# Kernel optimization log

Measured on AMD Instinct MI355X. Metric: run time of the kernel, lower is better.

The kernel has to match this reference:

```python
import jax, jax.numpy as jnp
import numpy as np

N, IN_DIM, HID, M, T, E, A, OUT = 10000, 256, 256, 8, 3, 160000, 2000, 10
LN_EPS = 1e-5


def _layernorm(x, g, b):
    mu = x.mean(-1, keepdims=True)
    var = ((x - mu) ** 2).mean(-1, keepdims=True)
    return (x - mu) * jax.lax.rsqrt(var + LN_EPS) * g + b


def _gcn_conv(x, w, b, src, dst, n):
    # PyG GCNConv: x' = D^{-1/2}(A+I)D^{-1/2} (x W) + b, deg counted on dst with self-loops
    xw = x @ w  # [n, out]
    loops = jnp.arange(n, dtype=src.dtype)
    s = jnp.concatenate([src, loops])
    d = jnp.concatenate([dst, loops])
    deg = jax.ops.segment_sum(jnp.ones(d.shape[0], xw.dtype), d, num_segments=n)
    dinv = jax.lax.rsqrt(jnp.maximum(deg, 1.0))
    norm = dinv[s] * dinv[d]
    out = jax.ops.segment_sum(xw[s] * norm[:, None], d, num_segments=n)
    return out + b


def setup_inputs() -> dict:
    key = jax.random.key(0)
    ks = jax.random.split(key, 26)
    g = lambda i, shape: (jax.random.normal(ks[i], shape, jnp.float32) * 0.02)
    return {
        "edge_index_t": jax.random.randint(ks[0], (T, 2, E), 0, N),
        "node_t": jax.random.randint(ks[1], (T, A), 0, N),
        "m": M,
        "emb": g(2, (N, IN_DIM)),
        "gcn_w1": g(3, (IN_DIM, HID)), "gcn_b1": jnp.zeros((HID,), jnp.float32),
        "gcn_w2": g(4, (HID, HID)), "gcn_b2": jnp.zeros((HID,), jnp.float32),
        "ln1_g": jnp.ones((HID,), jnp.float32), "ln1_b": jnp.zeros((HID,), jnp.float32),
        "tok_w1": g(5, (M, M)), "tok_b1": jnp.zeros((M,), jnp.float32),
        "tok_w2": g(6, (M, M)), "tok_b2": jnp.zeros((M,), jnp.float32),
        "ln2_g": jnp.ones((HID,), jnp.float32), "ln2_b": jnp.zeros((HID,), jnp.float32),
        "ch_w1": g(7, (HID, HID)), "ch_b1": jnp.zeros((HID,), jnp.float32),
        "ch_w2": g(8, (HID, HID)), "ch_b2": jnp.zeros((HID,), jnp.float32),
        "pred_w": g(9, (HID, HID)), "pred_b": jnp.zeros((HID,), jnp.float32),
        "cls1_w": g(10, (HID, HID)), "cls1_b": jnp.zeros((HID,), jnp.float32),
        "cls2_w": g(11, (HID, OUT)), "cls2_b": jnp.zeros((OUT,), jnp.float32),
    }


def reference(edge_index_t, node_t, m, emb,
              gcn_w1, gcn_b1, gcn_w2, gcn_b2,
              ln1_g, ln1_b, tok_w1, tok_b1, tok_w2, tok_b2,
              ln2_g, ln2_b, ch_w1, ch_b1, ch_w2, ch_b2,
              pred_w, pred_b, cls1_w, cls1_b, cls2_w, cls2_b):
    n = emb.shape[0]

    def mixer(xm):  # [n, m, hid]
        y = _layernorm(xm, ln1_g, ln1_b)
        # token MLP over the m axis (transpose(1,2) in torch)
        y = jnp.einsum('nmh,mk->nkh', y, tok_w1) + tok_b1[None, :, None]
        y = jax.nn.gelu(y, approximate=False)
        y = jnp.einsum('nmh,mk->nkh', y, tok_w2) + tok_b2[None, :, None]
        x = xm + y
        z = _layernorm(x, ln2_g, ln2_b)
        z = jax.nn.gelu(z @ ch_w1 + ch_b1, approximate=False) @ ch_w2 + ch_b2
        return x + z

    def step(x_m, inp):
        src, dst, nid = inp
        # forecast from current window (before this step's graph update)
        x_new = mixer(x_m).mean(axis=1)  # discrete FinalProcessLayer: mean over tokens
        # 2-layer GCN on the (shared) initial embeddings
        x = _gcn_conv(emb, gcn_w1, gcn_b1, src, dst, n)
        x = jax.nn.relu(x)
        x = _gcn_conv(x, gcn_w2, gcn_b2, src, dst, n)
        # boolean-mask scatter: zero rows of nodes listed in node_t[i]
        x = x.at[nid].set(0.0)
        x_m = jnp.concatenate([x_m[:, 1:, :], x[:, None, :]], axis=1)
        return x_m, x_new

    x_m0 = jnp.zeros((n, m, HID), emb.dtype)
    _, v = jax.lax.scan(step, x_m0, (edge_index_t[:, 0], edge_index_t[:, 1], node_t))
    # InvariantPredictor over all T timesteps at once: v [T, n, hid]
    h = jnp.tanh(v @ pred_w + pred_b)
    y_hat = jax.nn.relu((h @ cls1_w + cls1_b) @ cls2_w + cls2_b)
    return h, y_hat
```

## Files before the change

### kernel.cpp

```cpp
#include <hip/hip_runtime.h>
#include <math.h>

#define NN 10000
#define HIDD 256
#define MTOK 8
#define TT 3
#define EE 160000
#define AA 2000
#define OUTD 10
#define LNEPS 1e-5f

typedef unsigned short u16;
typedef __attribute__((ext_vector_type(8))) __bf16 bf16x8;
typedef __attribute__((ext_vector_type(4))) float f32x4;

__device__ __forceinline__ float gelu_f(float x) {
    return 0.5f * x * (1.f + erff(x * 0.7071067811865475f));
}
__device__ __forceinline__ u16 f2bf(float x) {
    unsigned u = __builtin_bit_cast(unsigned, x);
    return (u16)((u + 0x7FFFu + ((u >> 16) & 1u)) >> 16);
}
__device__ __forceinline__ float bf2f(u16 b) {
    return __builtin_bit_cast(float, (unsigned)b << 16);
}
__device__ __forceinline__ void gload16(const void* g, void* l) {
    __builtin_amdgcn_global_load_lds(
        (const __attribute__((address_space(1))) unsigned int*)g,
        (__attribute__((address_space(3))) unsigned int*)l, 16, 0, 0);
}

__global__ void count_kernel(const int* __restrict__ edge, int* __restrict__ cnt) {
    int g = blockIdx.y;
    const int* dst = edge + (size_t)g * 2 * EE + EE;
    int e = blockIdx.x * 256 + threadIdx.x;
    if (e < EE) atomicAdd(&cnt[g * NN + dst[e]], 1);
}

__global__ __launch_bounds__(1024) void scan_kernel(const int* __restrict__ cnt_all,
        int* __restrict__ rowstart_all, int* __restrict__ cursor_all, float* __restrict__ dinv_all) {
    int g = blockIdx.x;
    const int* cnt = cnt_all + (size_t)g * NN;
    int* rowstart = rowstart_all + (size_t)g * NN;
    int* cursor = cursor_all + (size_t)g * NN;
    float* dinv = dinv_all + (size_t)g * NN;
    __shared__ int wsum[16];
    int tid = threadIdx.x, lane = tid & 63, wid = tid >> 6;
    int carry = 0;
    for (int base = 0; base < NN; base += 1024) {
        int i = base + tid;
        int v = (i < NN) ? cnt[i] : 0;
        int s = v;
        #pragma unroll
        for (int o = 1; o < 64; o <<= 1) {
            int t = __shfl_up(s, o, 64);
            if (lane >= o) s += t;
        }
        if (lane == 63) wsum[wid] = s;
        __syncthreads();
        if (wid == 0) {
            int ws = (lane < 16) ? wsum[lane] : 0;
            #pragma unroll
            for (int o = 1; o < 16; o <<= 1) {
                int t = __shfl_up(ws, o, 64);
                if (lane >= o) ws += t;
            }
            if (lane < 16) wsum[lane] = ws;
        }
        __syncthreads();
        int woff = (wid > 0) ? wsum[wid - 1] : 0;
        int tot = wsum[15];
        if (i < NN) {
            int excl = carry + s + woff - v;
            rowstart[i] = excl;
            cursor[i] = excl;
            dinv[i] = rsqrtf((float)(v + 1));
        }
        carry += tot;
        __syncthreads();
    }
}

__global__ void fill_kernel(const int* __restrict__ edge, int* __restrict__ cursor, int* __restrict__ esrc) {
    int g = blockIdx.y;
    const int* src = edge + (size_t)g * 2 * EE;
    const int* dst = src + EE;
    int e = blockIdx.x * 256 + threadIdx.x;
    if (e < EE) {
        int d = dst[e];
        int idx = atomicAdd(&cursor[g * NN + d], 1);
        esrc[(size_t)g * EE + idx] = src[e];
    }
}

template<int RELU, int WF32, int WSPLIT>
__global__ __launch_bounds__(256) void gcn_agg(const float* __restrict__ xw, size_t xw_goff,
        const int* __restrict__ esrc_all, const int* __restrict__ rowstart_all,
        const int* __restrict__ cnt_all, const float* __restrict__ dinv_all,
        const float* __restrict__ bias, float* __restrict__ out,
        u16* __restrict__ ohi, u16* __restrict__ olo) {
    int g = blockIdx.y;
    const float* xwg = xw + (size_t)g * xw_goff;
    const int* esrc = esrc_all + (size_t)g * EE;
    const int* rowstart = rowstart_all + (size_t)g * NN;
    const int* cntp = cnt_all + (size_t)g * NN;
    const float* dinv = dinv_all + (size_t)g * NN;
    int wave = threadIdx.x >> 6, lane = threadIdx.x & 63;
    int d = blockIdx.x * 4 + wave;
    if (d >= NN) return;
    int start = rowstart[d];
    int len = cntp[d];
    float dd = dinv[d];
    int h = lane * 4;
    float4 a = *(const float4*)&xwg[(size_t)d * HIDD + h];
    float4 acc;
    acc.x = a.x * dd; acc.y = a.y * dd; acc.z = a.z * dd; acc.w = a.w * dd;
    for (int i = 0; i < len; i++) {
        int s = esrc[start + i];
        float ds = dinv[s];
        float4 b = *(const float4*)&xwg[(size_t)s * HIDD + h];
        acc.x = fmaf(b.x, ds, acc.x);
        acc.y = fmaf(b.y, ds, acc.y);
        acc.z = fmaf(b.z, ds, acc.z);
        acc.w = fmaf(b.w, ds, acc.w);
    }
    float o0 = acc.x * dd + bias[h + 0];
    float o1 = acc.y * dd + bias[h + 1];
    float o2 = acc.z * dd + bias[h + 2];
    float o3 = acc.w * dd + bias[h + 3];
    if (RELU) {
        o0 = fmaxf(o0, 0.f); o1 = fmaxf(o1, 0.f); o2 = fmaxf(o2, 0.f); o3 = fmaxf(o3, 0.f);
    }
    size_t obase = (size_t)g * NN * HIDD + (size_t)d * HIDD + h;
    if (WF32) {
        float4 o; o.x = o0; o.y = o1; o.z = o2; o.w = o3;
        *(float4*)&out[obase] = o;
    }
    if (WSPLIT) {
        ushort4 hv, lv;
        u16 h0 = f2bf(o0), h1 = f2bf(o1), h2 = f2bf(o2), h3 = f2bf(o3);
        hv.x = h0; hv.y = h1; hv.z = h2; hv.w = h3;
        lv.x = f2bf(o0 - bf2f(h0)); lv.y = f2bf(o1 - bf2f(h1));
        lv.z = f2bf(o2 - bf2f(h2)); lv.w = f2bf(o3 - bf2f(h3));
        *(ushort4*)&ohi[obase] = hv;
        *(ushort4*)&olo[obase] = lv;
    }
}

__global__ void mask_kernel(const int* __restrict__ node_t, float* __restrict__ xs) {
    int g = blockIdx.y;
    int node = node_t[(size_t)g * AA + blockIdx.x];
    xs[(size_t)g * NN * HIDD + (size_t)node * HIDD + threadIdx.x] = 0.f;
}

__global__ void split_kernel(const float* __restrict__ x, u16* __restrict__ hi, u16* __restrict__ lo, int n) {
    int i = blockIdx.x * 256 + threadIdx.x;
    if (i < n) {
        float v = x[i];
        u16 h = f2bf(v);
        hi[i] = h;
        lo[i] = f2bf(v - bf2f(h));
    }
}

__global__ void wsplit_all(const float* __restrict__ w0, const float* __restrict__ w1,
        const float* __restrict__ w2, const float* __restrict__ w3,
        const float* __restrict__ w4, const float* __restrict__ w5, u16* __restrict__ bt) {
    const float* W[6] = { w0, w1, w2, w3, w4, w5 };
    const float* Wm = W[blockIdx.y];
    u16* Bt = bt + (size_t)blockIdx.y * 256 * 768;
    int c = blockIdx.x, k = threadIdx.x;
    float x = Wm[k * 256 + c];
    u16 hi = f2bf(x), lo = f2bf(x - bf2f(hi));
    Bt[c * 768 + k] = hi;
    Bt[c * 768 + 256 + k] = hi;
    Bt[c * 768 + 512 + k] = lo;
}

template<int ACT, int WF32, int WSPLIT, int EPI>
__global__ __launch_bounds__(256) void gemm_split(
        const u16* __restrict__ Ahi, const u16* __restrict__ Alo,
        const u16* __restrict__ Bt, const float* __restrict__ bias,
        float* __restrict__ outf, u16* __restrict__ ohi, u16* __restrict__ olo,
        const float* __restrict__ xsum, int R) {
    __shared__ __align__(16) u16 ldsA[3][128 * 64];
    __shared__ __align__(16) u16 ldsB[2][128 * 64];
    int tid = threadIdx.x;
    int lane = tid & 63, w = tid >> 6;
    int nwg = gridDim.x, orig = blockIdx.x;
    int xcd = orig & 7, i8 = orig >> 3;
    int q = nwg >> 3, r = nwg & 7;
    int bid = (xcd < r ? xcd * (q + 1) : r * (q + 1) + (xcd - r) * q) + i8;
    int rowbase = (bid >> 1) * 128;
    int cb = bid & 1;
    int wrow = (w >> 1) * 64, wcol = (w & 1) * 64;
    f32x4 acc[4][4];
    #pragma unroll
    for (int i = 0; i < 4; i++)
        #pragma unroll
        for (int j = 0; j < 4; j++) acc[i][j] = f32x4{0.f, 0.f, 0.f, 0.f};

    constexpr int KCH[12]  = {0,4,1,5,2,6,3,7,8,9,10,11};
    constexpr int BNEW[12] = {1,0,1,0,1,0,1,0,1,1,1,1};
    constexpr int BBUF[12] = {0,0,1,1,0,0,1,1,0,1,0,1};
    constexpr int VMC[12]  = {8,12,8,12,8,12,8,12,12,12,8,0};

    auto stageA = [&](int slot, int c) {
        const u16* Aseg = (c >= 4 && c < 8) ? Alo : Ahi;
        int koff = (c & 3) * 64;
        #pragma unroll
        for (int i = 0; i < 4; i++) {
            int j = i * 256 + tid;
            int rr = j >> 3, sl = j & 7;
            int grow = rowbase + rr; if (grow > R - 1) grow = R - 1;
            const u16* gp = Aseg + (size_t)grow * 256 + koff + ((sl ^ (rr & 7)) << 3);
            gload16(gp, &ldsA[slot][(i * 256 + (tid & 192)) << 3]);
        }
    };
    auto stageB = [&](int buf, int c) {
        #pragma unroll
        for (int i = 0; i < 4; i++) {
            int j = i * 256 + tid;
            int rr = j >> 3, sl = j & 7;
            const u16* gp = Bt + (size_t)(cb * 128 + rr) * 768 + c * 64 + ((sl ^ (rr & 7)) << 3);
            gload16(gp, &ldsB[buf][(i * 256 + (tid & 192)) << 3]);
        }
    };

    stageB(0, KCH[0]);
    stageA(0, KCH[0]);
    stageA(1, KCH[1]);
    #pragma unroll
    for (int p = 0; p < 12; p++) {
        if (p + 1 <= 11 && BNEW[p + 1]) stageB(BBUF[p + 1], KCH[p + 1]);
        if (p + 2 <= 11) stageA((p + 2) % 3, KCH[p + 2]);
        if (VMC[p] == 12)      asm volatile("s_waitcnt vmcnt(12)" ::: "memory");
        else if (VMC[p] == 8)  asm volatile("s_waitcnt vmcnt(8)" ::: "memory");
        else                   asm volatile("s_waitcnt vmcnt(0)" ::: "memory");
        __builtin_amdgcn_s_barrier();
        __builtin_amdgcn_sched_barrier(0);
        __builtin_amdgcn_s_setprio(1);
        #pragma unroll
        for (int ks = 0; ks < 2; ks++) {
            bf16x8 a[4], b[4];
            #pragma unroll
            for (int rf = 0; rf < 4; rf++) {
                int rr = wrow + rf * 16 + (lane & 15);
                int slot = (lane >> 4) + ks * 4;
                a[rf] = *(const bf16x8*)&ldsA[p % 3][(rr << 6) + ((slot ^ (rr & 7)) << 3)];
            }
            #pragma unroll
            for (int cf = 0; cf < 4; cf++) {
                int cc = wcol + cf * 16 + (lane & 15);
                int slot = (lane >> 4) + ks * 4;
                b[cf] = *(const bf16x8*)&ldsB[BBUF[p]][(cc << 6) + ((slot ^ (cc & 7)) << 3)];
            }
            #pragma unroll
            for (int rf = 0; rf < 4; rf++)
                #pragma unroll
                for (int cf = 0; cf < 4; cf++)
                    acc[rf][cf] = __builtin_amdgcn_mfma_f32_16x16x32_bf16(a[rf], b[cf], acc[rf][cf], 0, 0, 0);
        }
        __builtin_amdgcn_s_setprio(0);
        __builtin_amdgcn_sched_barrier(0);
        __builtin_amdgcn_s_barrier();
    }
    #pragma unroll
    for (int rf = 0; rf < 4; rf++) {
        #pragma unroll
        for (int cf = 0; cf < 4; cf++) {
            int col = cb * 128 + wcol + cf * 16 + (lane & 15);
            float bv = bias[col];
            f32x4 v = acc[rf][cf];
            if (EPI == 1) {
                float s = 0.f;
                #pragma unroll
                for (int r2 = 0; r2 < 4; r2++) s += gelu_f(v[r2] + bv);
                float o = __shfl_xor(s, 16, 64);
                float nodesum = s + o;
                if (((lane >> 4) & 1) == 0) {
                    int node = ((rowbase + wrow + rf * 16) >> 3) + ((lane >> 4) >> 1);
                    u16 hi = f2bf(nodesum), lo = f2bf(nodesum - bf2f(hi));
                    ohi[(size_t)node * 256 + col] = hi;
                    olo[(size_t)node * 256 + col] = lo;
                }
            } else if (EPI == 2) {
                int row0 = rowbase + wrow + rf * 16 + ((lane >> 4) << 2);
                #pragma unroll
                for (int r2 = 0; r2 < 4; r2++) {
                    int row = row0 + r2;
                    if (row < R) {
                        float val = (xsum[(size_t)row * 256 + col] + v[r2] + 8.f * bv) * 0.125f;
                        u16 hi = f2bf(val), lo = f2bf(val - bf2f(hi));
                        ohi[(size_t)row * 256 + col] = hi;
                        olo[(size_t)row * 256 + col] = lo;
                    }
                }
            } else {
                int row0 = rowbase + wrow + rf * 16 + ((lane >> 4) << 2);
                #pragma unroll
                for (int r2 = 0; r2 < 4; r2++) {
                    int row = row0 + r2;
                    if (row < R) {
                        float val = v[r2] + bv;
                        if (ACT == 1) val = gelu_f(val);
                        if (ACT == 2) val = tanhf(val);
                        if (WF32) outf[(size_t)row * 256 + col] = val;
                        if (WSPLIT) {
                            u16 hi = f2bf(val), lo = f2bf(val - bf2f(hi));
                            ohi[(size_t)row * 256 + col] = hi;
                            olo[(size_t)row * 256 + col] = lo;
                        }
                    }
                }
            }
        }
    }
}

__global__ __launch_bounds__(256) void mixer_front(
        const float* __restrict__ xs, int nodebase,
        const float* __restrict__ ln1_g, const float* __restrict__ ln1_b,
        const float* __restrict__ tw1, const float* __restrict__ tb1,
        const float* __restrict__ tw2, const float* __restrict__ tb2,
        const float* __restrict__ ln2_g, const float* __restrict__ ln2_b,
        u16* __restrict__ z_hi, u16* __restrict__ z_lo, float* __restrict__ xsum_out) {
    int nv = nodebase + blockIdx.x;
    int step = nv >= NN ? 1 : 0;
    int n = nv - step * NN;
    const float* p1 = xs + ((size_t)step * NN + n) * HIDD;
    const float* p2 = step ? xs + (size_t)n * HIDD : nullptr;
    int tid = threadIdx.x;
    int wave = tid >> 6, lane = tid & 63;
    __shared__ __align__(16) float sx[MTOK][HIDD];
    __shared__ float stw1h[16], stw2[64], stb1[8], stb2[8], sw1s6[8];
    __shared__ float red[MTOK][2];
    if (tid < 16) stw1h[tid] = tw1[48 + tid];
    if (tid < 64) stw2[tid] = tw2[tid];
    if (tid < 8) {
        stb1[tid] = tb1[tid]; stb2[tid] = tb2[tid];
        float s = 0.f;
        #pragma unroll
        for (int m = 0; m < 6; m++) s += tw1[m * MTOK + tid];
        sw1s6[tid] = s;
    }
    sx[6][tid] = p2 ? p2[tid] : 0.f;
    sx[7][tid] = p1[tid];
    __syncthreads();
    float g1v = ln1_g[tid], b1v = ln1_b[tid];
    if (wave < 2) {
        int m = 6 + wave;
        float x0 = sx[m][lane], x1 = sx[m][lane + 64], x2 = sx[m][lane + 128], x3 = sx[m][lane + 192];
        float s = x0 + x1 + x2 + x3;
        float ss = x0 * x0 + x1 * x1 + x2 * x2 + x3 * x3;
        for (int off = 32; off > 0; off >>= 1) { s += __shfl_down(s, off, 64); ss += __shfl_down(ss, off, 64); }
        if (lane == 0) {
            float mu = s * (1.f / HIDD);
            float var = ss * (1.f / HIDD) - mu * mu;
            red[m][0] = mu;
            red[m][1] = rsqrtf(var + LNEPS);
        }
    }
    __syncthreads();
    float x6 = sx[6][tid], x7 = sx[7][tid];
    float ty6 = (x6 - red[6][0]) * red[6][1] * g1v + b1v;
    float ty7 = (x7 - red[7][0]) * red[7][1] * g1v + b1v;
    float u[MTOK];
    #pragma unroll
    for (int k = 0; k < MTOK; k++) {
        float a = stb1[k];
        a = fmaf(b1v, sw1s6[k], a);
        a = fmaf(ty6, stw1h[k], a);
        a = fmaf(ty7, stw1h[8 + k], a);
        u[k] = gelu_f(a);
    }
    float xsm = 0.f;
    #pragma unroll
    for (int k = 0; k < MTOK; k++) {
        float a = stb2[k];
        #pragma unroll
        for (int m = 0; m < MTOK; m++) a = fmaf(u[m], stw2[m * MTOK + k], a);
        if (k == 6) a += x6;
        if (k == 7) a += x7;
        sx[k][tid] = a;
        xsm += a;
    }
    xsum_out[(size_t)nv * HIDD + tid] = xsm;
    __syncthreads();
    float g2v = ln2_g[tid], b2v = ln2_b[tid];
    #pragma unroll
    for (int rep = 0; rep < 2; rep++) {
        int m = wave + rep * 4;
        float x0 = sx[m][lane], x1 = sx[m][lane + 64], x2 = sx[m][lane + 128], x3 = sx[m][lane + 192];
        float s = x0 + x1 + x2 + x3;
        float ss = x0 * x0 + x1 * x1 + x2 * x2 + x3 * x3;
        for (int off = 32; off > 0; off >>= 1) { s += __shfl_down(s, off, 64); ss += __shfl_down(ss, off, 64); }
        if (lane == 0) {
            float mu = s * (1.f / HIDD);
            float var = ss * (1.f / HIDD) - mu * mu;
            red[m][0] = mu;
            red[m][1] = rsqrtf(var + LNEPS);
        }
    }
    __syncthreads();
    #pragma unroll
    for (int m = 0; m < MTOK; m++) {
        float z = (sx[m][tid] - red[m][0]) * red[m][1] * g2v + b2v;
        u16 hi = f2bf(z), lo = f2bf(z - bf2f(hi));
        size_t idx = ((size_t)blockIdx.x * MTOK + m) * HIDD + tid;
        z_hi[idx] = hi;
        z_lo[idx] = lo;
    }
}

__global__ __launch_bounds__(256) void mixer_kernel(
        const float* __restrict__ ln1_g, const float* __restrict__ ln1_b,
        const float* __restrict__ tw1, const float* __restrict__ tb1,
        const float* __restrict__ tw2, const float* __restrict__ tb2,
        const float* __restrict__ ln2_g, const float* __restrict__ ln2_b,
        const float* __restrict__ cw1, const float* __restrict__ cb1,
        const float* __restrict__ cw2, const float* __restrict__ cb2,
        float* __restrict__ vout) {
    int tid = threadIdx.x;
    __shared__ __align__(16) float sx[MTOK][HIDD];
    __shared__ __align__(16) float sy[MTOK][HIDD];
    __shared__ float stw1[64], stw2[64], stb1[8], stb2[8];
    if (tid < 64) { stw1[tid] = tw1[tid]; stw2[tid] = tw2[tid]; }
    if (tid < 8)  { stb1[tid] = tb1[tid]; stb2[tid] = tb2[tid]; }
    __syncthreads();
    float b1v = ln1_b[tid];
    float ty[MTOK];
    #pragma unroll
    for (int m = 0; m < MTOK; m++) ty[m] = b1v;
    float u[MTOK];
    #pragma unroll
    for (int k = 0; k < MTOK; k++) {
        float a = stb1[k];
        #pragma unroll
        for (int m = 0; m < MTOK; m++) a = fmaf(ty[m], stw1[m * MTOK + k], a);
        u[k] = gelu_f(a);
    }
    #pragma unroll
    for (int k = 0; k < MTOK; k++) {
        float a = stb2[k];
        #pragma unroll
        for (int m = 0; m < MTOK; m++) a = fmaf(u[m], stw2[m * MTOK + k], a);
        sx[k][tid] = a;
    }
    __syncthreads();
    __shared__ float red[MTOK][2];
    int wave = tid >> 6, lane = tid & 63;
    float g2v = ln2_g[tid], b2v = ln2_b[tid];
    #pragma unroll
    for (int rep = 0; rep < 2; rep++) {
        int m = wave + rep * 4;
        float x0 = sx[m][lane], x1 = sx[m][lane + 64], x2 = sx[m][lane + 128], x3 = sx[m][lane + 192];
        float s = x0 + x1 + x2 + x3;
        float ss = x0 * x0 + x1 * x1 + x2 * x2 + x3 * x3;
        for (int off = 32; off > 0; off >>= 1) { s += __shfl_down(s, off, 64); ss += __shfl_down(ss, off, 64); }
        if (lane == 0) {
            float mu = s * (1.f / HIDD);
            float var = ss * (1.f / HIDD) - mu * mu;
            red[m][0] = mu;
            red[m][1] = rsqrtf(var + LNEPS);
        }
    }
    __syncthreads();
    #pragma unroll
    for (int m = 0; m < MTOK; m++) sy[m][tid] = (sx[m][tid] - red[m][0]) * red[m][1] * g2v + b2v;
    __syncthreads();
    float acc[MTOK];
    #pragma unroll
    for (int m = 0; m < MTOK; m++) acc[m] = 0.f;
    for (int h = 0; h < HIDD; h += 4) {
        float w0 = cw1[(h + 0) * HIDD + tid];
        float w1 = cw1[(h + 1) * HIDD + tid];
        float w2 = cw1[(h + 2) * HIDD + tid];
        float w3 = cw1[(h + 3) * HIDD + tid];
        #pragma unroll
        for (int m = 0; m < MTOK; m++) {
            const float4 a = *(const float4*)&sy[m][h];
            acc[m] = fmaf(a.x, w0, acc[m]);
            acc[m] = fmaf(a.y, w1, acc[m]);
            acc[m] = fmaf(a.z, w2, acc[m]);
            acc[m] = fmaf(a.w, w3, acc[m]);
        }
    }
    __syncthreads();
    float cb1v = cb1[tid];
    #pragma unroll
    for (int m = 0; m < MTOK; m++) sy[m][tid] = gelu_f(acc[m] + cb1v);
    __syncthreads();
    float acc2[MTOK];
    #pragma unroll
    for (int m = 0; m < MTOK; m++) acc2[m] = 0.f;
    for (int h = 0; h < HIDD; h += 4) {
        float w0 = cw2[(h + 0) * HIDD + tid];
        float w1 = cw2[(h + 1) * HIDD + tid];
        float w2 = cw2[(h + 2) * HIDD + tid];
        float w3 = cw2[(h + 3) * HIDD + tid];
        #pragma unroll
        for (int m = 0; m < MTOK; m++) {
            const float4 a = *(const float4*)&sy[m][h];
            acc2[m] = fmaf(a.x, w0, acc2[m]);
            acc2[m] = fmaf(a.y, w1, acc2[m]);
            acc2[m] = fmaf(a.z, w2, acc2[m]);
            acc2[m] = fmaf(a.w, w3, acc2[m]);
        }
    }
    float cb2v = cb2[tid];
    float ssum = 0.f;
    #pragma unroll
    for (int m = 0; m < MTOK; m++) ssum += sx[m][tid] + acc2[m] + cb2v;
    vout[tid] = ssum * (1.f / MTOK);
}

__global__ __launch_bounds__(256) void t0_head(const float* __restrict__ v0row,
        const float* __restrict__ pred_w, const float* __restrict__ pred_b,
        const float* __restrict__ cls1_w, const float* __restrict__ cls1_b,
        const float* __restrict__ cls2_w, const float* __restrict__ cls2_b,
        float* __restrict__ h0row, float* __restrict__ y0row) {
    __shared__ float s[HIDD], s2[HIDD];
    int tid = threadIdx.x;
    s[tid] = v0row[tid];
    __syncthreads();
    float a = 0.f;
    for (int k = 0; k < HIDD; k++) a = fmaf(s[k], pred_w[k * HIDD + tid], a);
    float h = tanhf(a + pred_b[tid]);
    h0row[tid] = h;
    s2[tid] = h;
    __syncthreads();
    a = 0.f;
    for (int k = 0; k < HIDD; k++) a = fmaf(s2[k], cls1_w[k * HIDD + tid], a);
    float g = a + cls1_b[tid];
    __syncthreads();
    s[tid] = g;
    __syncthreads();
    if (tid < OUTD) {
        float y = 0.f;
        for (int k = 0; k < HIDD; k++) y = fmaf(s[k], cls2_w[k * OUTD + tid], y);
        y0row[tid] = fmaxf(y + cls2_b[tid], 0.f);
    }
}

__global__ void bcast_both(const float* __restrict__ h0row, const float* __restrict__ y0row,
        float* __restrict__ hout, float* __restrict__ yout) {
    int n = blockIdx.x, tid = threadIdx.x;
    hout[(size_t)n * HIDD + tid] = h0row[tid];
    if (tid < OUTD) yout[(size_t)n * OUTD + tid] = y0row[tid];
}

__global__ __launch_bounds__(256) void cls2_kernel(const float* __restrict__ g1, const float* __restrict__ wm,
        const float* __restrict__ b, float* __restrict__ out, int rows) {
    __shared__ float sw[HIDD][12];
    int tid = threadIdx.x;
    for (int i = tid; i < HIDD * OUTD; i += 256) sw[i / OUTD][i % OUTD] = wm[i];
    __syncthreads();
    int rl = tid >> 4, kk = tid & 15;
    int r = blockIdx.x * 16 + rl;
    if (r < rows && kk < OUTD) {
        float acc = 0.f;
        const float* grow = g1 + (size_t)r * HIDD;
        for (int h = 0; h < HIDD; h++) acc = fmaf(grow[h], sw[h][kk], acc);
        out[(size_t)r * OUTD + kk] = fmaxf(acc + b[kk], 0.f);
    }
}

extern "C" void kernel_launch(void* const* d_in, const int* in_sizes, int n_in,
                              void* d_out, int out_size, void* d_ws, size_t ws_size,
                              hipStream_t stream) {
    const int* edge    = (const int*)d_in[0];
    const int* node_t  = (const int*)d_in[1];
    const float* emb   = (const float*)d_in[3];
    const float* gcn_w1 = (const float*)d_in[4];
    const float* gcn_b1 = (const float*)d_in[5];
    const float* gcn_w2 = (const float*)d_in[6];
    const float* gcn_b2 = (const float*)d_in[7];
    const float* ln1_g = (const float*)d_in[8];
    const float* ln1_b = (const float*)d_in[9];
    const float* tw1   = (const float*)d_in[10];
    const float* tb1   = (const float*)d_in[11];
    const float* tw2   = (const float*)d_in[12];
    const float* tb2   = (const float*)d_in[13];
    const float* ln2_g = (const float*)d_in[14];
    const float* ln2_b = (const float*)d_in[15];
    const float* cw1   = (const float*)d_in[16];
    const float* cb1   = (const float*)d_in[17];
    const float* cw2   = (const float*)d_in[18];
    const float* cb2   = (const float*)d_in[19];
    const float* pred_w = (const float*)d_in[20];
    const float* pred_b = (const float*)d_in[21];
    const float* cls1_w = (const float*)d_in[22];
    const float* cls1_b = (const float*)d_in[23];
    const float* cls2_w = (const float*)d_in[24];
    const float* cls2_b = (const float*)d_in[25];

    const size_t NH = (size_t)NN * HIDD;
    char* wsb = (char*)d_ws;
    size_t off = 0;
    auto alloc = [&](size_t bytes) { char* p = wsb + off; off = (off + bytes + 255) & ~(size_t)255; return p; };
    float* xs   = (float*)alloc(2 * NH * 4);
    u16* v_hi   = (u16*)alloc(2 * NH * 2);
    u16* v_lo   = (u16*)alloc(2 * NH * 2);
    u16* h_hi   = (u16*)alloc(2 * NH * 2);
    u16* h_lo   = (u16*)alloc(2 * NH * 2);
    float* xw2  = (float*)alloc(2 * NH * 4);
    float* xsum = (float*)alloc(2 * NH * 4);
    u16* Bt_all = (u16*)alloc((size_t)6 * 256 * 768 * 2);
    u16* Bt_cw1  = Bt_all;
    u16* Bt_cw2  = Bt_all + 1 * 256 * 768;
    u16* Bt_pred = Bt_all + 2 * 256 * 768;
    u16* Bt_cls1 = Bt_all + 3 * 256 * 768;
    u16* Bt_gw1  = Bt_all + 4 * 256 * 768;
    u16* Bt_gw2  = Bt_all + 5 * 256 * 768;
    float* dinv  = (float*)alloc(2 * NN * 4);
    float* zeros = (float*)alloc(HIDD * 4);
    float* v0row = (float*)alloc(HIDD * 4);
    float* h0row = (float*)alloc(HIDD * 4);
    float* y0row = (float*)alloc(16 * 4);
    int* cnt    = (int*)alloc(2 * NN * 4);
    int* rowst  = (int*)alloc(2 * NN * 4);
    int* cursor = (int*)alloc(2 * NN * 4);
    int* esrc   = (int*)alloc((size_t)2 * EE * 4);
    float* xw    = (float*)h_hi;
    u16*  emb_hi = h_lo;
    u16*  emb_lo = h_lo + NH;
    u16*  agg_hi = v_hi;
    u16*  agg_lo = v_lo;
    u16*  s2_hi  = (u16*)xw2;
    u16*  s2_lo  = (u16*)xw2 + 2 * NH;
    float* g1    = xw2;
    size_t remain = (ws_size > off + 4096) ? (ws_size - off - 4096) : 0;
    int CHN = (int)(remain / 8192);
    if (CHN > 2 * NN) CHN = 2 * NN;
    CHN &= ~15;
    if (CHN < 16) CHN = 16;
    const size_t ZE = (size_t)CHN * MTOK * HIDD;
    u16* z_hi  = (u16*)alloc(ZE * 2);
    u16* z_lo  = (u16*)alloc(ZE * 2);

    float* h_out = (float*)d_out;
    float* y_out = h_out + (size_t)TT * NH;

    hipMemsetAsync(zeros, 0, HIDD * sizeof(float), stream);
    wsplit_all<<<dim3(256, 6), 256, 0, stream>>>(cw1, cw2, pred_w, cls1_w, gcn_w1, gcn_w2, Bt_all);
    split_kernel<<<(NN * HIDD + 255) / 256, 256, 0, stream>>>(emb, emb_hi, emb_lo, NN * HIDD);
    gemm_split<0, 1, 0, 0><<<2 * ((NN + 127) / 128), 256, 0, stream>>>(
        emb_hi, emb_lo, Bt_gw1, zeros, xw, nullptr, nullptr, nullptr, NN);

    mixer_kernel<<<1, 256, 0, stream>>>(ln1_g, ln1_b, tw1, tb1, tw2, tb2,
        ln2_g, ln2_b, cw1, cb1, cw2, cb2, v0row);
    t0_head<<<1, 256, 0, stream>>>(v0row, pred_w, pred_b, cls1_w, cls1_b,
        cls2_w, cls2_b, h0row, y0row);
    bcast_both<<<NN, 256, 0, stream>>>(h0row, y0row, h_out, y_out);

    hipMemsetAsync(cnt, 0, 2 * NN * sizeof(int), stream);
    count_kernel<<<dim3((EE + 255) / 256, 2), 256, 0, stream>>>(edge, cnt);
    scan_kernel<<<2, 1024, 0, stream>>>(cnt, rowst, cursor, dinv);
    fill_kernel<<<dim3((EE + 255) / 256, 2), 256, 0, stream>>>(edge, cursor, esrc);
    gcn_agg<1, 0, 1><<<dim3((NN + 3) / 4, 2), 256, 0, stream>>>(xw, 0,
        esrc, rowst, cnt, dinv, gcn_b1, nullptr, agg_hi, agg_lo);
    gemm_split<0, 1, 0, 0><<<2 * ((2 * NN + 127) / 128), 256, 0, stream>>>(
        agg_hi, agg_lo, Bt_gw2, zeros, xw2, nullptr, nullptr, nullptr, 2 * NN);
    gcn_agg<0, 1, 0><<<dim3((NN + 3) / 4, 2), 256, 0, stream>>>(xw2, NH,
        esrc, rowst, cnt, dinv, gcn_b2, xs, nullptr, nullptr);
    mask_kernel<<<dim3(AA, 2), 256, 0, stream>>>(node_t, xs);

    for (int nb = 0; nb < 2 * NN; nb += CHN) {
        int nodes = 2 * NN - nb < CHN ? 2 * NN - nb : CHN;
        int R = nodes * MTOK;
        int rb = (R + 127) / 128;
        mixer_front<<<nodes, 256, 0, stream>>>(xs, nb,
            ln1_g, ln1_b, tw1, tb1, tw2, tb2, ln2_g, ln2_b, z_hi, z_lo, xsum);
        gemm_split<1, 0, 0, 1><<<2 * rb, 256, 0, stream>>>(
            z_hi, z_lo, Bt_cw1, cb1, nullptr,
            s2_hi + (size_t)nb * HIDD, s2_lo + (size_t)nb * HIDD, nullptr, R);
    }
    gemm_split<0, 0, 0, 2><<<2 * ((2 * NN + 127) / 128), 256, 0, stream>>>(
        s2_hi, s2_lo, Bt_cw2, cb2, nullptr, v_hi, v_lo, xsum, 2 * NN);
    gemm_split<2, 1, 1, 0><<<2 * ((2 * NN + 127) / 128), 256, 0, stream>>>(
        v_hi, v_lo, Bt_pred, pred_b,
        h_out + NH, h_hi, h_lo, nullptr, 2 * NN);
    gemm_split<0, 1, 0, 0><<<2 * ((2 * NN + 127) / 128), 256, 0, stream>>>(
        h_hi, h_lo, Bt_cls1, cls1_b, g1, nullptr, nullptr, nullptr, 2 * NN);
    cls2_kernel<<<(2 * NN + 15) / 16, 256, 0, stream>>>(g1, cls2_w, cls2_b, y_out + (size_t)NN * OUTD, 2 * NN);
}
```

Measured before the change: 550.6 us.

## Fuse channel-mix second GEMM, predictor, and classifier into one tail kernel

Replaces the last four launches (cw2 GEMM with mean epilogue, pred GEMM with tanh, cls1 GEMM, cls2 matvec) with one kernel. Each 64-row block keeps its activation tile in LDS as split bf16 hi/lo and chains the three 256x256 GEMMs while streaming weight chunks through double-buffered LDS. The cls2 projection then runs from LDS. This removes the global round trips for the intermediate activations and three launches. In exchange it uses large LDS (one block per CU), a smaller row tile, and recomputes weight staging per block.

```diff
diff --git a/kernel.cpp b/kernel.cpp
--- a/kernel.cpp
+++ b/kernel.cpp
@@ -284,18 +284,6 @@
                     ohi[(size_t)node * 256 + col] = hi;
                     olo[(size_t)node * 256 + col] = lo;
                 }
-            } else if (EPI == 2) {
-                int row0 = rowbase + wrow + rf * 16 + ((lane >> 4) << 2);
-                #pragma unroll
-                for (int r2 = 0; r2 < 4; r2++) {
-                    int row = row0 + r2;
-                    if (row < R) {
-                        float val = (xsum[(size_t)row * 256 + col] + v[r2] + 8.f * bv) * 0.125f;
-                        u16 hi = f2bf(val), lo = f2bf(val - bf2f(hi));
-                        ohi[(size_t)row * 256 + col] = hi;
-                        olo[(size_t)row * 256 + col] = lo;
-                    }
-                }
             } else {
                 int row0 = rowbase + wrow + rf * 16 + ((lane >> 4) << 2);
                 #pragma unroll
@@ -314,6 +302,132 @@
                     }
                 }
             }
+        }
+    }
+}
+
+__global__ __launch_bounds__(512, 1) void tail_fused(
+        const u16* __restrict__ s2_hi, const u16* __restrict__ s2_lo,
+        const float* __restrict__ xsum,
+        const u16* __restrict__ Bt_cw2, const float* __restrict__ cb2,
+        const u16* __restrict__ Bt_pred, const float* __restrict__ pred_b,
+        const u16* __restrict__ Bt_cls1, const float* __restrict__ cls1_b,
+        const float* __restrict__ cls2_w, const float* __restrict__ cls2_b,
+        float* __restrict__ h_out1, float* __restrict__ y_out1, int R) {
+    __shared__ __align__(16) u16 ldsA[2][64 * 256];
+    __shared__ __align__(16) u16 ldsB[2][256 * 64];
+    int tid = threadIdx.x;
+    int lane = tid & 63, wid = tid >> 6;
+    int wrow = (wid & 3) * 16, wcol = (wid >> 2) * 128;
+    int rowbase = blockIdx.x * 64;
+
+    constexpr int KCH[12]  = {0,4,1,5,2,6,3,7,8,9,10,11};
+    constexpr int BNEW[12] = {1,0,1,0,1,0,1,0,1,1,1,1};
+    constexpr int BBUF[12] = {0,0,1,1,0,0,1,1,0,1,0,1};
+
+    auto stageB = [&](int buf, int c, const u16* Bt) {
+        #pragma unroll
+        for (int i = 0; i < 4; i++) {
+            int j = i * 512 + tid;
+            int cc = j >> 3, sl = j & 7;
+            const u16* gp = Bt + (size_t)cc * 768 + c * 64 + ((sl ^ (cc & 7)) << 3);
+            gload16(gp, &ldsB[buf][(i * 512 + (tid & 448)) << 3]);
+        }
+    };
+    #pragma unroll
+    for (int seg = 0; seg < 2; seg++) {
+        const u16* src = seg ? s2_lo : s2_hi;
+        #pragma unroll
+        for (int i = 0; i < 4; i++) {
+            int j = i * 512 + tid;
+            int rr = j >> 5;
+            int gch = (j >> 3) & 3, t = j & 7;
+            int rowG = rowbase + rr; if (rowG > R - 1) rowG = R - 1;
+            const u16* gp = src + (size_t)rowG * 256 + gch * 64 + ((t ^ (rr & 7)) << 3);
+            gload16(gp, &ldsA[seg][(i * 512 + (tid & 448)) << 3]);
+        }
+    }
+
+    const u16* Bts0 = Bt_cw2;
+    const u16* Bts1 = Bt_pred;
+    const u16* Bts2 = Bt_cls1;
+    for (int s = 0; s < 3; s++) {
+        const u16* Bt = (s == 0) ? Bts0 : (s == 1) ? Bts1 : Bts2;
+        stageB(0, KCH[0], Bt);
+        asm volatile("s_waitcnt lgkmcnt(0)" ::: "memory");
+        __builtin_amdgcn_s_barrier();
+        f32x4 acc[8];
+        #pragma unroll
+        for (int i = 0; i < 8; i++) acc[i] = f32x4{0.f, 0.f, 0.f, 0.f};
+        #pragma unroll
+        for (int p = 0; p < 12; p++) {
+            if (p < 11 && BNEW[p + 1]) {
+                stageB(BBUF[p + 1], KCH[p + 1], Bt);
+                asm volatile("s_waitcnt vmcnt(4)" ::: "memory");
+            } else {
+                asm volatile("s_waitcnt vmcnt(0)" ::: "memory");
+            }
+            __builtin_amdgcn_s_barrier();
+            __builtin_amdgcn_sched_barrier(0);
+            __builtin_amdgcn_s_setprio(1);
+            int c = KCH[p];
+            int seg = (c >= 4 && c < 8) ? 1 : 0;
+            int kbase = (c & 3) * 64;
+            #pragma unroll
+            for (int ks = 0; ks < 2; ks++) {
+                int rr = wrow + (lane & 15);
+                int slot = (lane >> 4) + ks * 4;
+                bf16x8 a = *(const bf16x8*)&ldsA[seg][rr * 256 + kbase + ((slot ^ (rr & 7)) << 3)];
+                #pragma unroll
+                for (int cf = 0; cf < 8; cf++) {
+                    int cc = wcol + cf * 16 + (lane & 15);
+                    bf16x8 b = *(const bf16x8*)&ldsB[BBUF[p]][cc * 64 + ((slot ^ (cc & 7)) << 3)];
+                    acc[cf] = __builtin_amdgcn_mfma_f32_16x16x32_bf16(a, b, acc[cf], 0, 0, 0);
+                }
+            }
+            __builtin_amdgcn_s_setprio(0);
+            __builtin_amdgcn_sched_barrier(0);
+            __builtin_amdgcn_s_barrier();
+        }
+        #pragma unroll
+        for (int cf = 0; cf < 8; cf++) {
+            int col = wcol + cf * 16 + (lane & 15);
+            #pragma unroll
+            for (int r2 = 0; r2 < 4; r2++) {
+                int row = wrow + ((lane >> 4) << 2) + r2;
+                int rowG = rowbase + row;
+                int rowC = rowG > R - 1 ? R - 1 : rowG;
+                float av = acc[cf][r2];
+                int pos = row * 256 + (col >> 6) * 64 + ((((col >> 3) & 7) ^ (row & 7)) << 3) + (col & 7);
+                if (s == 0) {
+                    float val = (xsum[(size_t)rowC * 256 + col] + av + 8.f * cb2[col]) * 0.125f;
+                    u16 hi = f2bf(val), lo = f2bf(val - bf2f(hi));
+                    ldsA[0][pos] = hi;
+                    ldsA[1][pos] = lo;
+                } else if (s == 1) {
+                    float h = tanhf(av + pred_b[col]);
+                    if (rowG < R) h_out1[(size_t)rowG * 256 + col] = h;
+                    u16 hi = f2bf(h), lo = f2bf(h - bf2f(hi));
+                    ldsA[0][pos] = hi;
+                    ldsA[1][pos] = lo;
+                } else {
+                    ((float*)ldsA)[row * 256 + col] = av + cls1_b[col];
+                }
+            }
+        }
+    }
+    float* w2 = (float*)ldsB;
+    for (int i = tid; i < 256 * OUTD; i += 512) w2[i] = cls2_w[i];
+    asm volatile("s_waitcnt lgkmcnt(0) vmcnt(0)" ::: "memory");
+    __builtin_amdgcn_s_barrier();
+    const float* gbuf = (const float*)ldsA;
+    for (int o = tid; o < 64 * OUTD; o += 512) {
+        int row = o / OUTD, j = o - row * OUTD;
+        int rowG = rowbase + row;
+        if (rowG < R) {
+            float a2 = 0.f;
+            for (int k = 0; k < 256; k++) a2 = fmaf(gbuf[row * 256 + k], w2[k * OUTD + j], a2);
+            y_out1[(size_t)rowG * OUTD + j] = fmaxf(a2 + cls2_b[j], 0.f);
         }
     }
 }
@@ -548,22 +662,6 @@
     int n = blockIdx.x, tid = threadIdx.x;
     hout[(size_t)n * HIDD + tid] = h0row[tid];
     if (tid < OUTD) yout[(size_t)n * OUTD + tid] = y0row[tid];
-}
-
-__global__ __launch_bounds__(256) void cls2_kernel(const float* __restrict__ g1, const float* __restrict__ wm,
-        const float* __restrict__ b, float* __restrict__ out, int rows) {
-    __shared__ float sw[HIDD][12];
-    int tid = threadIdx.x;
-    for (int i = tid; i < HIDD * OUTD; i += 256) sw[i / OUTD][i % OUTD] = wm[i];
-    __syncthreads();
-    int rl = tid >> 4, kk = tid & 15;
-    int r = blockIdx.x * 16 + rl;
-    if (r < rows && kk < OUTD) {
-        float acc = 0.f;
-        const float* grow = g1 + (size_t)r * HIDD;
-        for (int h = 0; h < HIDD; h++) acc = fmaf(grow[h], sw[h][kk], acc);
-        out[(size_t)r * OUTD + kk] = fmaxf(acc + b[kk], 0.f);
-    }
 }
 
 extern "C" void kernel_launch(void* const* d_in, const int* in_sizes, int n_in,
@@ -629,7 +727,6 @@
     u16*  agg_lo = v_lo;
     u16*  s2_hi  = (u16*)xw2;
     u16*  s2_lo  = (u16*)xw2 + 2 * NH;
-    float* g1    = xw2;
     size_t remain = (ws_size > off + 4096) ? (ws_size - off - 4096) : 0;
     int CHN = (int)(remain / 8192);
     if (CHN > 2 * NN) CHN = 2 * NN;
@@ -676,12 +773,8 @@
             z_hi, z_lo, Bt_cw1, cb1, nullptr,
             s2_hi + (size_t)nb * HIDD, s2_lo + (size_t)nb * HIDD, nullptr, R);
     }
-    gemm_split<0, 0, 0, 2><<<2 * ((2 * NN + 127) / 128), 256, 0, stream>>>(
-        s2_hi, s2_lo, Bt_cw2, cb2, nullptr, v_hi, v_lo, xsum, 2 * NN);
-    gemm_split<2, 1, 1, 0><<<2 * ((2 * NN + 127) / 128), 256, 0, stream>>>(
-        v_hi, v_lo, Bt_pred, pred_b,
-        h_out + NH, h_hi, h_lo, nullptr, 2 * NN);
-    gemm_split<0, 1, 0, 0><<<2 * ((2 * NN + 127) / 128), 256, 0, stream>>>(
-        h_hi, h_lo, Bt_cls1, cls1_b, g1, nullptr, nullptr, nullptr, 2 * NN);
-    cls2_kernel<<<(2 * NN + 15) / 16, 256, 0, stream>>>(g1, cls2_w, cls2_b, y_out + (size_t)NN * OUTD, 2 * NN);
-}
+    tail_fused<<<(2 * NN + 63) / 64, 512, 0, stream>>>(
+        s2_hi, s2_lo, xsum,
+        Bt_cw2, cb2, Bt_pred, pred_b, Bt_cls1, cls1_b, cls2_w, cls2_b,
+        h_out + NH, y_out + (size_t)NN * OUTD, 2 * NN);
+}
```

Result: no change. 549.2 us (-0.2%).
